# Kernel tuning notes

Measured on AMD Instinct MI355X. Metric: run time of the kernel, lower is better.

Reference implementation:

```python
import jax, jax.numpy as jnp
import numpy as np

B, S, D, H, DH, F = 2, 2048, 1024, 16, 64, 4096
K = 2048  # number of selected tokens (capacity_gamma=0.5 of B*S)
EPS = 1e-6
ROPE_THETA = 10000.0


def setup_inputs() -> dict:
    key = jax.random.key(0)
    ks = jax.random.split(key, 12)
    w = lambda k, shp: jax.random.normal(k, shp, dtype=jnp.float32) * 0.02
    # K unique flat indices into the B*S token grid (every other token -> unique, sorted)
    sel_flat = jnp.arange(K, dtype=jnp.int64) * 2
    return {
        "hidden_states": jax.random.normal(ks[0], (B, S, D), dtype=jnp.float32),
        "gating_signal": jax.random.uniform(ks[1], (B, S), dtype=jnp.float32),
        "sel_flat": sel_flat,
        "position_ids": jnp.tile(jnp.arange(S, dtype=jnp.int64), (B, 1)),
        "ln1_w": jnp.ones((D,), jnp.float32),
        "ln2_w": jnp.ones((D,), jnp.float32),
        "wq": w(ks[2], (D, H * DH)), "bq": jnp.zeros((H * DH,), jnp.float32),
        "wk": w(ks[3], (D, H * DH)), "bk": jnp.zeros((H * DH,), jnp.float32),
        "wv": w(ks[4], (D, H * DH)), "bv": jnp.zeros((H * DH,), jnp.float32),
        "wo": w(ks[5], (H * DH, D)),
        "w_gate": w(ks[6], (D, F)),
        "w_up": w(ks[7], (D, F)),
        "w_down": w(ks[8], (F, D)),
    }


def _rmsnorm(x, w):
    var = jnp.mean(jnp.square(x), axis=-1, keepdims=True)
    return x * jax.lax.rsqrt(var + EPS) * w


def _rope(x, pos):
    # x: [K, H, DH], pos: [K]
    half = DH // 2
    inv_freq = 1.0 / (ROPE_THETA ** (jnp.arange(half, dtype=jnp.float32) / half))
    ang = pos.astype(jnp.float32)[:, None] * inv_freq  # [K, half]
    cos = jnp.cos(ang)[:, None, :]
    sin = jnp.sin(ang)[:, None, :]
    x1, x2 = x[..., :half], x[..., half:]
    return jnp.concatenate([x1 * cos - x2 * sin, x2 * cos + x1 * sin], axis=-1)


def reference(hidden_states, gating_signal, sel_flat, position_ids,
              ln1_w, ln2_w, wq, bq, wk, bk, wv, bv, wo, w_gate, w_up, w_down):
    b_idx = sel_flat // S
    t_idx = sel_flat % S

    # --- gather selected tokens ---
    x = hidden_states[b_idx, t_idx]          # [K, D]
    g = gating_signal[b_idx, t_idx]          # [K]
    pos = position_ids[b_idx, t_idx]         # [K]

    # --- Qwen2 block on the selected tokens (single sequence of length K) ---
    h = _rmsnorm(x, ln1_w)
    q = _rope((h @ wq + bq).reshape(K, H, DH), pos)
    k = _rope((h @ wk + bk).reshape(K, H, DH), pos)
    v = (h @ wv + bv).reshape(K, H, DH)

    scores = jnp.einsum("qhd,khd->hqk", q, k) / np.sqrt(DH)  # [H, K, K]
    causal = jnp.tril(jnp.ones((K, K), dtype=bool))
    scores = jnp.where(causal, scores, jnp.finfo(scores.dtype).min)
    probs = jax.nn.softmax(scores, axis=-1)
    attn = jnp.einsum("hqk,khd->qhd", probs, v).reshape(K, H * DH) @ wo

    x1 = x + attn
    h2 = _rmsnorm(x1, ln2_w)
    mlp = (jax.nn.silu(h2 @ w_gate) * (h2 @ w_up)) @ w_down
    y = x1 + mlp                              # processed tokens [K, D]

    # --- gated residual scatter-back ---
    updated = x + (y - x) * g[:, None]
    return hidden_states.at[b_idx, t_idx].set(updated)
```

## Files before the change

### kernel.cpp

```cpp
#include <hip/hip_runtime.h>
#include <hip/hip_bf16.h>
#include <stdint.h>

#define K_TOK 2048
#define D_DIM 1024
#define H_N   16
#define DH_N  64
#define F_DIM 4096
#define S_SEQ 2048

typedef __attribute__((ext_vector_type(4))) float f32x4;
typedef __attribute__((ext_vector_type(8))) short bf16x8;

__device__ __forceinline__ float bf2f(ushort u) {
  union { unsigned u; float f; } c; c.u = ((unsigned)u) << 16; return c.f;
}
__device__ __forceinline__ ushort f2bf(float f) {
  union { float f; unsigned u; } c; c.f = f;
  unsigned x = c.u + 0x7fffu + ((c.u >> 16) & 1u);
  return (ushort)(x >> 16);
}

#define GLOAD_LDS16(GP, LP)                                                   \
  __builtin_amdgcn_global_load_lds(                                           \
      (const __attribute__((address_space(1))) unsigned int*)(GP),            \
      (__attribute__((address_space(3))) unsigned int*)(LP), 16, 0, 0)

__global__ void copy_out_k(const float4* __restrict__ src, float4* __restrict__ dst, int n4) {
  int idx = blockIdx.x * blockDim.x + threadIdx.x;
  int stride = gridDim.x * blockDim.x;
  for (; idx < n4; idx += stride) dst[idx] = src[idx];
}

__global__ void prep_bias(const float* __restrict__ bq, const float* __restrict__ bk,
                          const float* __restrict__ bv, float* __restrict__ dst) {
  int i = blockIdx.x * 256 + threadIdx.x;
  if (i < 3072) dst[i] = (i < 1024) ? bq[i] : (i < 2048 ? bk[i - 1024] : bv[i - 2048]);
}

__global__ __launch_bounds__(256) void transpose_conv64(const float* __restrict__ src,
                                                        ushort* __restrict__ dst,
                                                        int R, int C, int mul, int add, int ldd) {
  __shared__ float tile[64][65];
  int nbx = C >> 6;
  int bx = blockIdx.x % nbx, by = blockIdx.x / nbx;
  int c0 = bx << 6, r0 = by << 6;
  int tx = threadIdx.x & 15, ty = threadIdx.x >> 4;
#pragma unroll
  for (int i = 0; i < 4; ++i) {
    float4 v = *(const float4*)&src[(size_t)(r0 + ty + i * 16) * C + c0 + tx * 4];
    *(float4*)&tile[ty + i * 16][tx * 4] = v;
  }
  __syncthreads();
#pragma unroll
  for (int i = 0; i < 4; ++i) {
    int c = ty + i * 16;
    ushort4 o;
    o.x = f2bf(tile[tx * 4 + 0][c]);
    o.y = f2bf(tile[tx * 4 + 1][c]);
    o.z = f2bf(tile[tx * 4 + 2][c]);
    o.w = f2bf(tile[tx * 4 + 3][c]);
    *(ushort4*)&dst[(size_t)((c0 + c) * mul + add) * ldd + r0 + tx * 4] = o;
  }
}

__global__ __launch_bounds__(256) void gather_ln1(
    const float* __restrict__ hs, const float* __restrict__ gating,
    const int* __restrict__ sel32, const int* __restrict__ pos32,
    const float* __restrict__ w,
    float* __restrict__ xbuf, ushort* __restrict__ hbuf,
    float* __restrict__ gbuf, int* __restrict__ rowb, int* __restrict__ rowt,
    int* __restrict__ rowpos) {
  int i = blockIdx.x, tid = threadIdx.x;
  __shared__ float red[4];
  bool is64 = (sel32[1] == 0 && sel32[3] == 0 && sel32[5] == 0);
  int sel = is64 ? sel32[2 * i] : sel32[i];
  int b = sel >> 11;
  int t = sel & 2047;
  const float4* src = (const float4*)(hs + ((size_t)b * S_SEQ + t) * D_DIM);
  float4 v = src[tid];
  float ss = v.x * v.x + v.y * v.y + v.z * v.z + v.w * v.w;
  for (int off = 32; off; off >>= 1) ss += __shfl_xor(ss, off);
  if ((tid & 63) == 0) red[tid >> 6] = ss;
  __syncthreads();
  float tot = red[0] + red[1] + red[2] + red[3];
  float rms = rsqrtf(tot * (1.f / 1024.f) + 1e-6f);
  ((float4*)(xbuf + (size_t)i * D_DIM))[tid] = v;
  float4 lw = ((const float4*)w)[tid];
  ushort4 hv;
  hv.x = f2bf(v.x * rms * lw.x); hv.y = f2bf(v.y * rms * lw.y);
  hv.z = f2bf(v.z * rms * lw.z); hv.w = f2bf(v.w * rms * lw.w);
  *(ushort4*)&hbuf[(size_t)i * D_DIM + tid * 4] = hv;
  if (tid == 0) {
    rowb[i] = b; rowt[i] = t;
    bool is64p = (pos32[1] == 0 && pos32[3] == 0 && pos32[5] == 0);
    int pidx = b * S_SEQ + t;
    rowpos[i] = is64p ? pos32[2 * pidx] : pos32[pidx];
    gbuf[i] = gating[pidx];
  }
}

__global__ __launch_bounds__(256) void rmsnorm_ep1(const float* __restrict__ xbuf,
                                                   const float* __restrict__ pb,
                                                   const float* __restrict__ w,
                                                   float* __restrict__ x1out,
                                                   ushort* __restrict__ h2out) {
  int i = blockIdx.x, tid = threadIdx.x;
  __shared__ float red[4];
  size_t e = (size_t)i * D_DIM;
  float4 v = ((const float4*)(xbuf + e))[tid];
  float4 p0 = ((const float4*)(pb + e))[tid];
  float4 p1 = ((const float4*)(pb + 2097152 + e))[tid];
  v.x += p0.x + p1.x; v.y += p0.y + p1.y; v.z += p0.z + p1.z; v.w += p0.w + p1.w;
  ((float4*)(x1out + e))[tid] = v;
  float ss = v.x * v.x + v.y * v.y + v.z * v.z + v.w * v.w;
  for (int off = 32; off; off >>= 1) ss += __shfl_xor(ss, off);
  if ((tid & 63) == 0) red[tid >> 6] = ss;
  __syncthreads();
  float tot = red[0] + red[1] + red[2] + red[3];
  float rms = rsqrtf(tot * (1.f / 1024.f) + 1e-6f);
  float4 lw = ((const float4*)w)[tid];
  ushort4 hv;
  hv.x = f2bf(v.x * rms * lw.x); hv.y = f2bf(v.y * rms * lw.y);
  hv.z = f2bf(v.z * rms * lw.z); hv.w = f2bf(v.w * rms * lw.w);
  *(ushort4*)&h2out[e + tid * 4] = hv;
}

__global__ __launch_bounds__(256) void ep3_k(const float* __restrict__ pb,
                                             const float* __restrict__ x1b,
                                             const float* __restrict__ xbuf,
                                             const float* __restrict__ gbuf,
                                             const int* __restrict__ rowb,
                                             const int* __restrict__ rowt,
                                             float* __restrict__ out) {
  int idx = blockIdx.x * 256 + threadIdx.x;
  int row = idx >> 8, c4 = idx & 255;
  size_t e = (size_t)row * D_DIM + c4 * 4;
  float4 s0 = *(const float4*)(pb + e);
  float4 s1 = *(const float4*)(pb + 2097152 + e);
  float4 s2 = *(const float4*)(pb + 2 * 2097152 + e);
  float4 s3 = *(const float4*)(pb + 3 * 2097152 + e);
  float4 x = *(const float4*)(xbuf + e);
  float4 x1 = *(const float4*)(x1b + e);
  float g = gbuf[row];
  float4 r;
  r.x = x.x + (x1.x + s0.x + s1.x + s2.x + s3.x - x.x) * g;
  r.y = x.y + (x1.y + s0.y + s1.y + s2.y + s3.y - x.y) * g;
  r.z = x.z + (x1.z + s0.z + s1.z + s2.z + s3.z - x.z) * g;
  r.w = x.w + (x1.w + s0.w + s1.w + s2.w + s3.w - x.w) * g;
  *(float4*)(out + ((size_t)rowb[row] * S_SEQ + rowt[row]) * D_DIM + c4 * 4) = r;
}

template <int MODE>
__global__ __launch_bounds__(256) void gemm_bt(
    const ushort* __restrict__ A, const ushort* __restrict__ BT,
    int M, int N, int ldk, int kdeff, int per,
    const float* __restrict__ bias,
    ushort* __restrict__ outb, float* __restrict__ outf) {
  __shared__ ushort lA[128 * 64];
  __shared__ ushort lB[128 * 64];
  int tid = threadIdx.x;
  int lane = tid & 63, wid = tid >> 6;
  int kidx = blockIdx.x / per;
  int bid = blockIdx.x % per;
  int nbn = N >> 7;
  int tm = bid / nbn, tn = bid % nbn;
  int wr = wid >> 1, wc = wid & 1;
  f32x4 acc[4][4];
#pragma unroll
  for (int m = 0; m < 4; ++m)
#pragma unroll
    for (int n = 0; n < 4; ++n) acc[m][n] = (f32x4){0.f, 0.f, 0.f, 0.f};

  const ushort* Ab = A + (size_t)(tm * 128) * ldk + (size_t)kidx * kdeff;
  const ushort* Bb = BT + (size_t)(tn * 128) * ldk + (size_t)kidx * kdeff;
  int lr = lane & 15, lg = lane >> 4;
  int prow = lane >> 3;
  int pch = lane & 7;

  for (int k0 = 0; k0 < kdeff; k0 += 64) {
    __syncthreads();
#pragma unroll
    for (int p = 0; p < 4; ++p) {
      int row = p * 32 + wid * 8 + prow;
      int g = pch ^ (row & 7);
      GLOAD_LDS16(Ab + (size_t)row * ldk + k0 + g * 8, &lA[(p * 32 + wid * 8) * 64]);
      GLOAD_LDS16(Bb + (size_t)row * ldk + k0 + g * 8, &lB[(p * 32 + wid * 8) * 64]);
    }
    __syncthreads();
#pragma unroll
    for (int ks = 0; ks < 2; ++ks) {
      bf16x8 af[4], bfv[4];
#pragma unroll
      for (int m = 0; m < 4; ++m) {
        int row = wr * 64 + m * 16 + lr;
        af[m] = *(const bf16x8*)((const char*)lA + row * 128 +
                                 ((ks * 64 + lg * 16) ^ ((row & 7) << 4)));
      }
#pragma unroll
      for (int n = 0; n < 4; ++n) {
        int row = wc * 64 + n * 16 + lr;
        bfv[n] = *(const bf16x8*)((const char*)lB + row * 128 +
                                  ((ks * 64 + lg * 16) ^ ((row & 7) << 4)));
      }
#pragma unroll
      for (int m = 0; m < 4; ++m)
#pragma unroll
        for (int n = 0; n < 4; ++n)
          acc[m][n] = __builtin_amdgcn_mfma_f32_16x16x32_bf16(af[m], bfv[n], acc[m][n], 0, 0, 0);
    }
  }

#pragma unroll
  for (int m = 0; m < 4; ++m) {
#pragma unroll
    for (int n = 0; n < 4; ++n) {
#pragma unroll
      for (int r = 0; r < 4; ++r) {
        int gr = tm * 128 + wr * 64 + m * 16 + lg * 4 + r;
        int gc = tn * 128 + wc * 64 + n * 16 + lr;
        float val = acc[m][n][r];
        if (MODE == 0) {
          outb[(size_t)gr * N + gc] = f2bf(val + bias[gc]);
        } else {
          outf[((size_t)kidx * M + gr) * N + gc] = val;
        }
      }
    }
  }
}

__global__ __launch_bounds__(512, 2) void gemm256_gu(const ushort* __restrict__ A,
                                                     const ushort* __restrict__ BT,
                                                     ushort* __restrict__ outb) {
  __shared__ ushort lA[2][256 * 64];
  __shared__ ushort lB[2][256 * 64];
  int tid = threadIdx.x, lane = tid & 63, wid = tid >> 6;
  int bid = blockIdx.x;
  int tm = bid & 7, tn = bid >> 3;
  int wm = wid >> 2, wn = wid & 3;
  int lr = lane & 15, lg = lane >> 4;
  const ushort* Ab = A + (size_t)(tm * 256) * 1024;
  const ushort* Bb = BT + (size_t)(tn * 256) * 1024;

  f32x4 acc[8][4];
#pragma unroll
  for (int m = 0; m < 8; ++m)
#pragma unroll
    for (int n = 0; n < 4; ++n) acc[m][n] = (f32x4){0.f, 0.f, 0.f, 0.f};

  int grow = lane >> 3;
  int gsw = (lane & 7) ^ grow;

  auto STG = [&](int bi, int t) {
#pragma unroll
    for (int r = 0; r < 4; ++r) {
      int rb = wid * 4 + r;
      int row = rb * 8 + grow;
      GLOAD_LDS16(Ab + (size_t)row * 1024 + t * 64 + gsw * 8, &lA[bi][rb * 512]);
      GLOAD_LDS16(Bb + (size_t)row * 1024 + t * 64 + gsw * 8, &lB[bi][rb * 512]);
    }
  };

  STG(0, 0);
  STG(1, 1);
  asm volatile("s_waitcnt vmcnt(8)" ::: "memory");
  __builtin_amdgcn_s_barrier();

  for (int t = 0; t < 16; ++t) {
    int c = t & 1;
    const char* bA = (const char*)&lA[c][0];
    const char* bB = (const char*)&lB[c][0];
    bf16x8 bfr[4][2], afh[4][2];
#pragma unroll
    for (int n = 0; n < 4; ++n) {
      int row = wn * 64 + n * 16 + lr;
#pragma unroll
      for (int kk = 0; kk < 2; ++kk)
        bfr[n][kk] = *(const bf16x8*)(bB + row * 128 + ((kk * 64 + lg * 16) ^ ((lr & 7) << 4)));
    }
#pragma unroll
    for (int m = 0; m < 4; ++m) {
      int row = wm * 128 + m * 16 + lr;
#pragma unroll
      for (int kk = 0; kk < 2; ++kk)
        afh[m][kk] = *(const bf16x8*)(bA + row * 128 + ((kk * 64 + lg * 16) ^ ((lr & 7) << 4)));
    }
    __builtin_amdgcn_s_setprio(1);
#pragma unroll
    for (int m = 0; m < 4; ++m)
#pragma unroll
      for (int n = 0; n < 4; ++n)
#pragma unroll
        for (int kk = 0; kk < 2; ++kk)
          acc[m][n] = __builtin_amdgcn_mfma_f32_16x16x32_bf16(afh[m][kk], bfr[n][kk],
                                                              acc[m][n], 0, 0, 0);
    __builtin_amdgcn_s_setprio(0);
#pragma unroll
    for (int m = 0; m < 4; ++m) {
      int row = wm * 128 + 64 + m * 16 + lr;
#pragma unroll
      for (int kk = 0; kk < 2; ++kk)
        afh[m][kk] = *(const bf16x8*)(bA + row * 128 + ((kk * 64 + lg * 16) ^ ((lr & 7) << 4)));
    }
    asm volatile("s_waitcnt lgkmcnt(0)" ::: "memory");
    __builtin_amdgcn_s_barrier();
    if (t + 2 < 16) STG(c, t + 2);
    __builtin_amdgcn_sched_barrier(0);
    __builtin_amdgcn_s_setprio(1);
#pragma unroll
    for (int m = 0; m < 4; ++m)
#pragma unroll
      for (int n = 0; n < 4; ++n)
#pragma unroll
        for (int kk = 0; kk < 2; ++kk)
          acc[4 + m][n] = __builtin_amdgcn_mfma_f32_16x16x32_bf16(afh[m][kk], bfr[n][kk],
                                                                  acc[4 + m][n], 0, 0, 0);
    __builtin_amdgcn_s_setprio(0);
    if (t < 15) {
      if (t + 2 < 16)
        asm volatile("s_waitcnt vmcnt(8)" ::: "memory");
      else
        asm volatile("s_waitcnt vmcnt(0)" ::: "memory");
      __builtin_amdgcn_s_barrier();
    }
  }

#pragma unroll
  for (int m = 0; m < 8; ++m) {
#pragma unroll
    for (int n = 0; n < 4; ++n) {
#pragma unroll
      for (int r = 0; r < 4; ++r) {
        int gr = tm * 256 + wm * 128 + m * 16 + lg * 4 + r;
        int gc = tn * 256 + wn * 64 + n * 16 + lr;
        float val = acc[m][n][r];
        float other = __shfl_xor(val, 1);
        if (!(lane & 1)) {
          float g = val, u = other;
          float a = g / (1.f + __expf(-g)) * u;
          outb[(size_t)gr * (F_DIM) + (gc >> 1)] = f2bf(a);
        }
      }
    }
  }
}

__global__ __launch_bounds__(256) void rope_kernel(const ushort* __restrict__ qkv,
                                                   const int* __restrict__ rowpos,
                                                   ushort* __restrict__ qr,
                                                   ushort* __restrict__ kr) {
  int idx = blockIdx.x * 256 + threadIdx.x;
  int i = idx >> 9;
  int rem = idx & 511;
  int h = rem >> 5, d = rem & 31;
  float pos = (float)rowpos[i];
  float inv = __expf(-(float)d * (9.210340371976184f / 32.0f));
  float ang = pos * inv;
  float sn, cs;
  __sincosf(ang, &sn, &cs);
  size_t base = (size_t)i * 3072;
  float q1 = bf2f(qkv[base + h * 64 + d]);
  float q2 = bf2f(qkv[base + h * 64 + 32 + d]);
  float k1 = bf2f(qkv[base + 1024 + h * 64 + d]);
  float k2 = bf2f(qkv[base + 1024 + h * 64 + 32 + d]);
  size_t ob = ((size_t)h * K_TOK + i) * DH_N;
  qr[ob + d] = f2bf((q1 * cs - q2 * sn) * 0.125f);
  qr[ob + 32 + d] = f2bf((q2 * cs + q1 * sn) * 0.125f);
  kr[ob + d] = f2bf(k1 * cs - k2 * sn);
  kr[ob + 32 + d] = f2bf(k2 * cs + k1 * sn);
}

__global__ __launch_bounds__(256) void vtrans_k(const ushort* __restrict__ qkv,
                                                ushort* __restrict__ vt) {
  __shared__ ushort tile[32][33];
  int bx = blockIdx.x & 63, by = blockIdx.x >> 6;
  int i0 = bx << 5, c0 = by << 5;
  int tx = threadIdx.x & 31, ty = threadIdx.x >> 5;
#pragma unroll
  for (int j = 0; j < 32; j += 8)
    tile[ty + j][tx] = qkv[(size_t)(i0 + ty + j) * 3072 + 2048 + c0 + tx];
  __syncthreads();
#pragma unroll
  for (int j = 0; j < 32; j += 8)
    vt[(size_t)(c0 + ty + j) * K_TOK + i0 + tx] = tile[tx][ty + j];
}

__global__ __launch_bounds__(256) void attn_mfma(const ushort* __restrict__ qr,
                                                 const ushort* __restrict__ kr,
                                                 const ushort* __restrict__ vt,
                                                 ushort* __restrict__ ows,
                                                 float* __restrict__ mlws) {
  __shared__ ushort ktile[2][64 * 64];
  __shared__ ushort vtile[2][64 * 64];
  __shared__ ushort pbuf[4][16 * 64];
  int tid = threadIdx.x, lane = tid & 63, wid = tid >> 6;
  int bid = blockIdx.x;
  int h = bid / 144;
  int rem = 143 - (bid % 144);
  int g = 0;
  while (rem >= 2 * (g + 1) * (g + 2)) ++g;
  int rem2 = rem - 2 * g * (g + 1);
  int qt = (g << 2) + rem2 / (g + 1);
  int ci = rem2 % (g + 1);
  int slot = h * 144 + rem;
  int q0 = qt << 6;
  int t0 = ci << 2;
  int t1 = min(t0 + 3, qt);

  const ushort* Kh = kr + (size_t)h * K_TOK * DH_N;
  const ushort* Vh = vt + (size_t)h * DH_N * K_TOK;
  int lr = lane & 15, lg = lane >> 4;
  int qbase = q0 + wid * 16;

  bf16x8 qf[2];
  const ushort* Qp = qr + ((size_t)h * K_TOK + qbase + lr) * DH_N + lg * 8;
  qf[0] = *(const bf16x8*)(Qp);
  qf[1] = *(const bf16x8*)(Qp + 32);

  f32x4 oa[4];
  float mreg[4], lreg[4];
#pragma unroll
  for (int ct = 0; ct < 4; ++ct) oa[ct] = (f32x4){0.f, 0.f, 0.f, 0.f};
#pragma unroll
  for (int r = 0; r < 4; ++r) { mreg[r] = -1e30f; lreg[r] = 0.f; }

  char* pws = (char*)&pbuf[wid][0];
  int srow8 = lane >> 3, schunk = lane & 7;

  auto stage = [&](int bi, int kb) {
#pragma unroll
    for (int j = 0; j < 2; ++j) {
      int rbase = wid * 16 + j * 8;
      int row = rbase + srow8;
      int gch = schunk ^ (row & 7);
      GLOAD_LDS16(Kh + (size_t)(kb + row) * DH_N + gch * 8, &ktile[bi][rbase * 64]);
      GLOAD_LDS16(Vh + (size_t)row * K_TOK + kb + gch * 8, &vtile[bi][rbase * 64]);
    }
  };

  stage(0, t0 << 6);
  int cur = 0;
  for (int t = t0; t <= t1; ++t) {
    int kb = t << 6;
    __syncthreads();
    if (t < t1) stage(cur ^ 1, (t + 1) << 6);

    const char* kt = (const char*)&ktile[cur][0];
    const char* vtl = (const char*)&vtile[cur][0];

    f32x4 sa[4];
#pragma unroll
    for (int ct = 0; ct < 4; ++ct) sa[ct] = (f32x4){0.f, 0.f, 0.f, 0.f};
#pragma unroll
    for (int s = 0; s < 2; ++s) {
#pragma unroll
      for (int ct = 0; ct < 4; ++ct) {
        int row = ct * 16 + lr;
        bf16x8 kf = *(const bf16x8*)(kt + row * 128 + ((s * 64 + lg * 16) ^ ((row & 7) << 4)));
        sa[ct] = __builtin_amdgcn_mfma_f32_16x16x32_bf16(qf[s], kf, sa[ct], 0, 0, 0);
      }
    }

#pragma unroll
    for (int r = 0; r < 4; ++r) {
      int q = qbase + lg * 4 + r;
      int prow = lg * 4 + r;
      float sv[4];
      float mx = mreg[r];
#pragma unroll
      for (int ct = 0; ct < 4; ++ct) {
        int key = kb + ct * 16 + lr;
        float x = sa[ct][r];
        sv[ct] = (key <= q) ? x : -1e30f;
        mx = fmaxf(mx, sv[ct]);
      }
      mx = fmaxf(mx, __shfl_xor(mx, 1));
      mx = fmaxf(mx, __shfl_xor(mx, 2));
      mx = fmaxf(mx, __shfl_xor(mx, 4));
      mx = fmaxf(mx, __shfl_xor(mx, 8));
      float resc = __expf(mreg[r] - mx);
      float ps = 0.f;
#pragma unroll
      for (int ct = 0; ct < 4; ++ct) {
        float p = __expf(sv[ct] - mx);
        ps += p;
        *(ushort*)(pws + prow * 128 + ((ct * 32 + lr * 2) ^ ((prow & 7) << 4))) = f2bf(p);
      }
      ps += __shfl_xor(ps, 1);
      ps += __shfl_xor(ps, 2);
      ps += __shfl_xor(ps, 4);
      ps += __shfl_xor(ps, 8);
      lreg[r] = lreg[r] * resc + ps;
      mreg[r] = mx;
#pragma unroll
      for (int ct = 0; ct < 4; ++ct) oa[ct][r] *= resc;
    }

    bf16x8 pf[2];
#pragma unroll
    for (int s = 0; s < 2; ++s)
      pf[s] = *(const bf16x8*)(pws + lr * 128 + ((s * 64 + lg * 16) ^ ((lr & 7) << 4)));
#pragma unroll
    for (int s = 0; s < 2; ++s) {
#pragma unroll
      for (int ct = 0; ct < 4; ++ct) {
        int row = ct * 16 + lr;
        bf16x8 vf = *(const bf16x8*)(vtl + row * 128 + ((s * 64 + lg * 16) ^ ((row & 7) << 4)));
        oa[ct] = __builtin_amdgcn_mfma_f32_16x16x32_bf16(pf[s], vf, oa[ct], 0, 0, 0);
      }
    }
    cur ^= 1;
  }

#pragma unroll
  for (int ct = 0; ct < 4; ++ct) {
#pragma unroll
    for (int r = 0; r < 4; ++r) {
      int prow = wid * 16 + lg * 4 + r;
      ows[(size_t)slot * 4096 + prow * 64 + ct * 16 + lr] = f2bf(oa[ct][r]);
    }
  }
  if (lr == 0) {
#pragma unroll
    for (int r = 0; r < 4; ++r) {
      int prow = wid * 16 + lg * 4 + r;
      mlws[(size_t)slot * 128 + prow] = mreg[r];
      mlws[(size_t)slot * 128 + 64 + prow] = lreg[r];
    }
  }
}

__global__ __launch_bounds__(256) void attn_combine(const ushort* __restrict__ ows,
                                                    const float* __restrict__ mlws,
                                                    ushort* __restrict__ aout) {
  int bid = blockIdx.x;
  int h = bid & 15, qt = bid >> 4;
  int g = qt >> 2;
  int nc = g + 1;
  int base = h * 144 + 2 * g * (g + 1) + (qt & 3) * nc;
  int tid = threadIdx.x;
  int row = tid >> 2, c0 = (tid & 3) * 16;
  float M = -1e30f;
  for (int i = 0; i < nc; ++i)
    M = fmaxf(M, mlws[(size_t)(base + i) * 128 + row]);
  float L = 0.f;
  float acc[16];
#pragma unroll
  for (int j = 0; j < 16; ++j) acc[j] = 0.f;
  for (int i = 0; i < nc; ++i) {
    size_t sl = (size_t)(base + i);
    float w = __expf(mlws[sl * 128 + row] - M);
    L += mlws[sl * 128 + 64 + row] * w;
    const bf16x8* op = (const bf16x8*)(ows + sl * 4096 + row * 64 + c0);
    bf16x8 v0 = op[0], v1 = op[1];
#pragma unroll
    for (int j = 0; j < 8; ++j) acc[j] += bf2f(((ushort)v0[j])) * w;
#pragma unroll
    for (int j = 0; j < 8; ++j) acc[8 + j] += bf2f(((ushort)v1[j])) * w;
  }
  float inv = 1.f / L;
  int q = qt * 64 + row;
  ushort* dst = aout + (size_t)q * D_DIM + h * DH_N + c0;
#pragma unroll
  for (int j = 0; j < 16; ++j) dst[j] = f2bf(acc[j] * inv);
}

extern "C" void kernel_launch(void* const* d_in, const int* in_sizes, int n_in,
                              void* d_out, int out_size, void* d_ws, size_t ws_size,
                              hipStream_t stream) {
  const float* hs = (const float*)d_in[0];
  const float* gating = (const float*)d_in[1];
  const int* sel32 = (const int*)d_in[2];
  const int* pos32 = (const int*)d_in[3];
  const float* ln1w = (const float*)d_in[4];
  const float* ln2w = (const float*)d_in[5];
  const float* wq = (const float*)d_in[6];
  const float* bq = (const float*)d_in[7];
  const float* wk = (const float*)d_in[8];
  const float* bk = (const float*)d_in[9];
  const float* wv = (const float*)d_in[10];
  const float* bv = (const float*)d_in[11];
  const float* wo = (const float*)d_in[12];
  const float* wg = (const float*)d_in[13];
  const float* wu = (const float*)d_in[14];
  const float* wd = (const float*)d_in[15];
  float* out = (float*)d_out;

  char* wsb = (char*)d_ws;
  size_t off = 0;
  auto alloc = [&](size_t bytes) -> void* {
    void* p = wsb + off;
    off += (bytes + 255) & ~(size_t)255;
    return p;
  };
  ushort* qkvT = (ushort*)alloc(3072ull * 1024 * 2);
  ushort* woT = (ushort*)alloc(1024ull * 1024 * 2);
  ushort* guT = (ushort*)alloc(8192ull * 1024 * 2);
  ushort* wdT = (ushort*)alloc(1024ull * 4096 * 2);
  float* biasqkv = (float*)alloc(3072 * 4);
  float* xbuf = (float*)alloc(2048ull * 1024 * 4);
  ushort* hbuf = (ushort*)alloc(2048ull * 1024 * 2);
  ushort* qkv = (ushort*)alloc(2048ull * 3072 * 2);
  ushort* qrb = (ushort*)alloc(16ull * 2048 * 64 * 2);
  ushort* krb = (ushort*)alloc(16ull * 2048 * 64 * 2);
  ushort* vtb = (ushort*)alloc(16ull * 64 * 2048 * 2);
  ushort* aoutb = (ushort*)alloc(2048ull * 1024 * 2);
  float* pbuf = (float*)hbuf;
  float* x1b = (float*)alloc(2048ull * 1024 * 4);
  ushort* h2b = (ushort*)alloc(2048ull * 1024 * 2);
  ushort* actb = (ushort*)alloc(2048ull * 4096 * 2);
  ushort* aows = (ushort*)x1b;
  float* amlws = (float*)((char*)x1b + 2304ull * 4096 * 2);
  float* gbuf = (float*)alloc(2048 * 4);
  int* rowb = (int*)alloc(2048 * 4);
  int* rowt = (int*)alloc(2048 * 4);
  int* rowpos = (int*)alloc(2048 * 4);
  if (off > ws_size) return;

  copy_out_k<<<2048, 256, 0, stream>>>((const float4*)hs, (float4*)out, (2 * S_SEQ * D_DIM) / 4);
  prep_bias<<<12, 256, 0, stream>>>(bq, bk, bv, biasqkv);
  transpose_conv64<<<256, 256, 0, stream>>>(wq, qkvT, 1024, 1024, 1, 0, 1024);
  transpose_conv64<<<256, 256, 0, stream>>>(wk, qkvT + 1024 * 1024, 1024, 1024, 1, 0, 1024);
  transpose_conv64<<<256, 256, 0, stream>>>(wv, qkvT + 2048 * 1024, 1024, 1024, 1, 0, 1024);
  transpose_conv64<<<256, 256, 0, stream>>>(wo, woT, 1024, 1024, 1, 0, 1024);
  transpose_conv64<<<1024, 256, 0, stream>>>(wg, guT, 1024, 4096, 2, 0, 1024);
  transpose_conv64<<<1024, 256, 0, stream>>>(wu, guT, 1024, 4096, 2, 1, 1024);
  transpose_conv64<<<1024, 256, 0, stream>>>(wd, wdT, 4096, 1024, 1, 0, 4096);
  gather_ln1<<<2048, 256, 0, stream>>>(hs, gating, sel32, pos32, ln1w, xbuf, hbuf, gbuf, rowb,
                                       rowt, rowpos);
  gemm_bt<0><<<16 * 24, 256, 0, stream>>>(hbuf, qkvT, 2048, 3072, 1024, 1024, 16 * 24, biasqkv,
                                          qkv, nullptr);
  rope_kernel<<<4096, 256, 0, stream>>>(qkv, rowpos, qrb, krb);
  vtrans_k<<<2048, 256, 0, stream>>>(qkv, vtb);
  attn_mfma<<<16 * 144, 256, 0, stream>>>(qrb, krb, vtb, aows, amlws);
  attn_combine<<<512, 256, 0, stream>>>(aows, amlws, aoutb);
  gemm_bt<4><<<2 * 16 * 8, 256, 0, stream>>>(aoutb, woT, 2048, 1024, 1024, 512, 16 * 8, nullptr,
                                             nullptr, pbuf);
  rmsnorm_ep1<<<2048, 256, 0, stream>>>(xbuf, pbuf, ln2w, x1b, h2b);
  gemm256_gu<<<256, 512, 0, stream>>>(h2b, guT, actb);
  gemm_bt<4><<<4 * 16 * 8, 256, 0, stream>>>(actb, wdT, 2048, 1024, 4096, 1024, 16 * 8, nullptr,
                                             nullptr, pbuf);
  ep3_k<<<2048, 256, 0, stream>>>(pbuf, x1b, xbuf, gbuf, rowb, rowt, out);
}
```

Measured before the change: 218.6 us.

## Merge prep launches, double-buffer gemm_bt LDS, remap gate/up tile order

Folds the seven weight-transpose launches and the bias packing into one prep_all kernel. It also merges the output copy with gather/LN1 and RoPE with the V transpose, which removes several kernel launches and their tail gaps. gemm_bt now uses double-buffered LDS with async global-to-LDS prefetch two tiles ahead, split-k MFMA phases and setprio, so loads overlap with compute. The gemm256_gu block-to-tile mapping is changed, apparently to improve L2 reuse. The cost is double the LDS in gemm_bt, which may lower occupancy, plus more complex waitcnt logic.

```diff
diff --git a/kernel.cpp b/kernel.cpp
--- a/kernel.cpp
+++ b/kernel.cpp
@@ -26,24 +26,38 @@
       (const __attribute__((address_space(1))) unsigned int*)(GP),            \
       (__attribute__((address_space(3))) unsigned int*)(LP), 16, 0, 0)
 
-__global__ void copy_out_k(const float4* __restrict__ src, float4* __restrict__ dst, int n4) {
-  int idx = blockIdx.x * blockDim.x + threadIdx.x;
-  int stride = gridDim.x * blockDim.x;
-  for (; idx < n4; idx += stride) dst[idx] = src[idx];
-}
-
-__global__ void prep_bias(const float* __restrict__ bq, const float* __restrict__ bk,
-                          const float* __restrict__ bv, float* __restrict__ dst) {
-  int i = blockIdx.x * 256 + threadIdx.x;
-  if (i < 3072) dst[i] = (i < 1024) ? bq[i] : (i < 2048 ? bk[i - 1024] : bv[i - 2048]);
-}
-
-__global__ __launch_bounds__(256) void transpose_conv64(const float* __restrict__ src,
-                                                        ushort* __restrict__ dst,
-                                                        int R, int C, int mul, int add, int ldd) {
+__global__ __launch_bounds__(256) void prep_all(
+    const float* __restrict__ wq, const float* __restrict__ wk,
+    const float* __restrict__ wv, const float* __restrict__ wo,
+    const float* __restrict__ wg, const float* __restrict__ wu,
+    const float* __restrict__ wd, const float* __restrict__ bq,
+    const float* __restrict__ bk, const float* __restrict__ bv,
+    ushort* __restrict__ qkvT, ushort* __restrict__ woT,
+    ushort* __restrict__ guT, ushort* __restrict__ wdT,
+    float* __restrict__ biasqkv) {
   __shared__ float tile[64][65];
+  int b = blockIdx.x;
+  if (b >= 4096) {
+    int i = (b - 4096) * 256 + threadIdx.x;
+    if (i < 3072)
+      biasqkv[i] = (i < 1024) ? bq[i] : (i < 2048 ? bk[i - 1024] : bv[i - 2048]);
+    return;
+  }
+  const float* src;
+  ushort* dst;
+  int C, mul, add, ldd, tid_tile;
+  if (b < 1024) {
+    int seg = b >> 8; tid_tile = b & 255; C = 1024; mul = 1; add = 0; ldd = 1024;
+    if (seg == 0) { src = wq; dst = qkvT; }
+    else if (seg == 1) { src = wk; dst = qkvT + 1024 * 1024; }
+    else if (seg == 2) { src = wv; dst = qkvT + 2048 * 1024; }
+    else { src = wo; dst = woT; }
+  } else if (b < 2048) { src = wg; dst = guT; tid_tile = b - 1024; C = 4096; mul = 2; add = 0; ldd = 1024; }
+  else if (b < 3072) { src = wu; dst = guT; tid_tile = b - 2048; C = 4096; mul = 2; add = 1; ldd = 1024; }
+  else { src = wd; dst = wdT; tid_tile = b - 3072; C = 1024; mul = 1; add = 0; ldd = 4096; }
+
   int nbx = C >> 6;
-  int bx = blockIdx.x % nbx, by = blockIdx.x / nbx;
+  int bx = tid_tile % nbx, by = tid_tile / nbx;
   int c0 = bx << 6, r0 = by << 6;
   int tx = threadIdx.x & 15, ty = threadIdx.x >> 4;
 #pragma unroll
@@ -64,15 +78,21 @@
   }
 }
 
-__global__ __launch_bounds__(256) void gather_ln1(
+__global__ __launch_bounds__(256) void gather_copy(
     const float* __restrict__ hs, const float* __restrict__ gating,
     const int* __restrict__ sel32, const int* __restrict__ pos32,
-    const float* __restrict__ w,
+    const float* __restrict__ w, float* __restrict__ outc,
     float* __restrict__ xbuf, ushort* __restrict__ hbuf,
     float* __restrict__ gbuf, int* __restrict__ rowb, int* __restrict__ rowt,
     int* __restrict__ rowpos) {
-  int i = blockIdx.x, tid = threadIdx.x;
   __shared__ float red[4];
+  int tid = threadIdx.x;
+  if (blockIdx.x < 4096) {
+    int idx = blockIdx.x * 256 + tid;
+    ((float4*)outc)[idx] = ((const float4*)hs)[idx];
+    return;
+  }
+  int i = blockIdx.x - 4096;
   bool is64 = (sel32[1] == 0 && sel32[3] == 0 && sel32[5] == 0);
   int sel = is64 ? sel32[2 * i] : sel32[i];
   int b = sel >> 11;
@@ -157,8 +177,8 @@
     int M, int N, int ldk, int kdeff, int per,
     const float* __restrict__ bias,
     ushort* __restrict__ outb, float* __restrict__ outf) {
-  __shared__ ushort lA[128 * 64];
-  __shared__ ushort lB[128 * 64];
+  __shared__ ushort lA[2][128 * 64];
+  __shared__ ushort lB[2][128 * 64];
   int tid = threadIdx.x;
   int lane = tid & 63, wid = tid >> 6;
   int kidx = blockIdx.x / per;
@@ -177,37 +197,70 @@
   int lr = lane & 15, lg = lane >> 4;
   int prow = lane >> 3;
   int pch = lane & 7;
-
-  for (int k0 = 0; k0 < kdeff; k0 += 64) {
-    __syncthreads();
+  int nk = kdeff >> 6;
+
+  auto STG = [&](int bi, int t) {
 #pragma unroll
     for (int p = 0; p < 4; ++p) {
-      int row = p * 32 + wid * 8 + prow;
+      int rb = p * 32 + wid * 8;
+      int row = rb + prow;
       int g = pch ^ (row & 7);
-      GLOAD_LDS16(Ab + (size_t)row * ldk + k0 + g * 8, &lA[(p * 32 + wid * 8) * 64]);
-      GLOAD_LDS16(Bb + (size_t)row * ldk + k0 + g * 8, &lB[(p * 32 + wid * 8) * 64]);
-    }
-    __syncthreads();
-#pragma unroll
-    for (int ks = 0; ks < 2; ++ks) {
-      bf16x8 af[4], bfv[4];
-#pragma unroll
-      for (int m = 0; m < 4; ++m) {
-        int row = wr * 64 + m * 16 + lr;
-        af[m] = *(const bf16x8*)((const char*)lA + row * 128 +
-                                 ((ks * 64 + lg * 16) ^ ((row & 7) << 4)));
-      }
-#pragma unroll
-      for (int n = 0; n < 4; ++n) {
-        int row = wc * 64 + n * 16 + lr;
-        bfv[n] = *(const bf16x8*)((const char*)lB + row * 128 +
-                                  ((ks * 64 + lg * 16) ^ ((row & 7) << 4)));
-      }
-#pragma unroll
-      for (int m = 0; m < 4; ++m)
-#pragma unroll
-        for (int n = 0; n < 4; ++n)
-          acc[m][n] = __builtin_amdgcn_mfma_f32_16x16x32_bf16(af[m], bfv[n], acc[m][n], 0, 0, 0);
+      GLOAD_LDS16(Ab + (size_t)row * ldk + t * 64 + g * 8, &lA[bi][rb * 64]);
+      GLOAD_LDS16(Bb + (size_t)row * ldk + t * 64 + g * 8, &lB[bi][rb * 64]);
+    }
+  };
+
+  STG(0, 0);
+  STG(1, 1);
+  asm volatile("s_waitcnt vmcnt(8)" ::: "memory");
+  __builtin_amdgcn_s_barrier();
+
+  for (int t = 0; t < nk; ++t) {
+    int c = t & 1;
+    const char* bA = (const char*)&lA[c][0];
+    const char* bB = (const char*)&lB[c][0];
+    bf16x8 bfv[4][2], af[4];
+#pragma unroll
+    for (int n = 0; n < 4; ++n) {
+      int row = wc * 64 + n * 16 + lr;
+#pragma unroll
+      for (int kk = 0; kk < 2; ++kk)
+        bfv[n][kk] = *(const bf16x8*)(bB + row * 128 + ((kk * 64 + lg * 16) ^ ((row & 7) << 4)));
+    }
+#pragma unroll
+    for (int m = 0; m < 4; ++m) {
+      int row = wr * 64 + m * 16 + lr;
+      af[m] = *(const bf16x8*)(bA + row * 128 + ((lg * 16) ^ ((row & 7) << 4)));
+    }
+    __builtin_amdgcn_s_setprio(1);
+#pragma unroll
+    for (int m = 0; m < 4; ++m)
+#pragma unroll
+      for (int n = 0; n < 4; ++n)
+        acc[m][n] = __builtin_amdgcn_mfma_f32_16x16x32_bf16(af[m], bfv[n][0], acc[m][n], 0, 0, 0);
+    __builtin_amdgcn_s_setprio(0);
+#pragma unroll
+    for (int m = 0; m < 4; ++m) {
+      int row = wr * 64 + m * 16 + lr;
+      af[m] = *(const bf16x8*)(bA + row * 128 + ((64 + lg * 16) ^ ((row & 7) << 4)));
+    }
+    asm volatile("s_waitcnt lgkmcnt(0)" ::: "memory");
+    __builtin_amdgcn_s_barrier();
+    if (t + 2 < nk) STG(c, t + 2);
+    __builtin_amdgcn_sched_barrier(0);
+    __builtin_amdgcn_s_setprio(1);
+#pragma unroll
+    for (int m = 0; m < 4; ++m)
+#pragma unroll
+      for (int n = 0; n < 4; ++n)
+        acc[m][n] = __builtin_amdgcn_mfma_f32_16x16x32_bf16(af[m], bfv[n][1], acc[m][n], 0, 0, 0);
+    __builtin_amdgcn_s_setprio(0);
+    if (t < nk - 1) {
+      if (t + 2 < nk)
+        asm volatile("s_waitcnt vmcnt(8)" ::: "memory");
+      else
+        asm volatile("s_waitcnt vmcnt(0)" ::: "memory");
+      __builtin_amdgcn_s_barrier();
     }
   }
 
@@ -237,7 +290,8 @@
   __shared__ ushort lB[2][256 * 64];
   int tid = threadIdx.x, lane = tid & 63, wid = tid >> 6;
   int bid = blockIdx.x;
-  int tm = bid & 7, tn = bid >> 3;
+  int tn = (bid & 7) * 4 + ((bid >> 3) & 3);
+  int tm = bid >> 5;
   int wm = wid >> 2, wn = wid & 3;
   int lr = lane & 15, lg = lane >> 4;
   const ushort* Ab = A + (size_t)(tm * 256) * 1024;
@@ -346,35 +400,36 @@
   }
 }
 
-__global__ __launch_bounds__(256) void rope_kernel(const ushort* __restrict__ qkv,
+__global__ __launch_bounds__(256) void rope_vtrans(const ushort* __restrict__ qkv,
                                                    const int* __restrict__ rowpos,
                                                    ushort* __restrict__ qr,
-                                                   ushort* __restrict__ kr) {
-  int idx = blockIdx.x * 256 + threadIdx.x;
-  int i = idx >> 9;
-  int rem = idx & 511;
-  int h = rem >> 5, d = rem & 31;
-  float pos = (float)rowpos[i];
-  float inv = __expf(-(float)d * (9.210340371976184f / 32.0f));
-  float ang = pos * inv;
-  float sn, cs;
-  __sincosf(ang, &sn, &cs);
-  size_t base = (size_t)i * 3072;
-  float q1 = bf2f(qkv[base + h * 64 + d]);
-  float q2 = bf2f(qkv[base + h * 64 + 32 + d]);
-  float k1 = bf2f(qkv[base + 1024 + h * 64 + d]);
-  float k2 = bf2f(qkv[base + 1024 + h * 64 + 32 + d]);
-  size_t ob = ((size_t)h * K_TOK + i) * DH_N;
-  qr[ob + d] = f2bf((q1 * cs - q2 * sn) * 0.125f);
-  qr[ob + 32 + d] = f2bf((q2 * cs + q1 * sn) * 0.125f);
-  kr[ob + d] = f2bf(k1 * cs - k2 * sn);
-  kr[ob + 32 + d] = f2bf(k2 * cs + k1 * sn);
-}
-
-__global__ __launch_bounds__(256) void vtrans_k(const ushort* __restrict__ qkv,
-                                                ushort* __restrict__ vt) {
+                                                   ushort* __restrict__ kr,
+                                                   ushort* __restrict__ vt) {
   __shared__ ushort tile[32][33];
-  int bx = blockIdx.x & 63, by = blockIdx.x >> 6;
+  if (blockIdx.x < 4096) {
+    int idx = blockIdx.x * 256 + threadIdx.x;
+    int i = idx >> 9;
+    int rem = idx & 511;
+    int h = rem >> 5, d = rem & 31;
+    float pos = (float)rowpos[i];
+    float inv = __expf(-(float)d * (9.210340371976184f / 32.0f));
+    float ang = pos * inv;
+    float sn, cs;
+    __sincosf(ang, &sn, &cs);
+    size_t base = (size_t)i * 3072;
+    float q1 = bf2f(qkv[base + h * 64 + d]);
+    float q2 = bf2f(qkv[base + h * 64 + 32 + d]);
+    float k1 = bf2f(qkv[base + 1024 + h * 64 + d]);
+    float k2 = bf2f(qkv[base + 1024 + h * 64 + 32 + d]);
+    size_t ob = ((size_t)h * K_TOK + i) * DH_N;
+    qr[ob + d] = f2bf((q1 * cs - q2 * sn) * 0.125f);
+    qr[ob + 32 + d] = f2bf((q2 * cs + q1 * sn) * 0.125f);
+    kr[ob + d] = f2bf(k1 * cs - k2 * sn);
+    kr[ob + 32 + d] = f2bf(k2 * cs + k1 * sn);
+    return;
+  }
+  int bid = blockIdx.x - 4096;
+  int bx = bid & 63, by = bid >> 6;
   int i0 = bx << 5, c0 = by << 5;
   int tx = threadIdx.x & 31, ty = threadIdx.x >> 5;
 #pragma unroll
@@ -618,21 +673,13 @@
   int* rowpos = (int*)alloc(2048 * 4);
   if (off > ws_size) return;
 
-  copy_out_k<<<2048, 256, 0, stream>>>((const float4*)hs, (float4*)out, (2 * S_SEQ * D_DIM) / 4);
-  prep_bias<<<12, 256, 0, stream>>>(bq, bk, bv, biasqkv);
-  transpose_conv64<<<256, 256, 0, stream>>>(wq, qkvT, 1024, 1024, 1, 0, 1024);
-  transpose_conv64<<<256, 256, 0, stream>>>(wk, qkvT + 1024 * 1024, 1024, 1024, 1, 0, 1024);
-  transpose_conv64<<<256, 256, 0, stream>>>(wv, qkvT + 2048 * 1024, 1024, 1024, 1, 0, 1024);
-  transpose_conv64<<<256, 256, 0, stream>>>(wo, woT, 1024, 1024, 1, 0, 1024);
-  transpose_conv64<<<1024, 256, 0, stream>>>(wg, guT, 1024, 4096, 2, 0, 1024);
-  transpose_conv64<<<1024, 256, 0, stream>>>(wu, guT, 1024, 4096, 2, 1, 1024);
-  transpose_conv64<<<1024, 256, 0, stream>>>(wd, wdT, 4096, 1024, 1, 0, 4096);
-  gather_ln1<<<2048, 256, 0, stream>>>(hs, gating, sel32, pos32, ln1w, xbuf, hbuf, gbuf, rowb,
-                                       rowt, rowpos);
+  prep_all<<<4108, 256, 0, stream>>>(wq, wk, wv, wo, wg, wu, wd, bq, bk, bv, qkvT, woT, guT,
+                                     wdT, biasqkv);
+  gather_copy<<<6144, 256, 0, stream>>>(hs, gating, sel32, pos32, ln1w, out, xbuf, hbuf, gbuf,
+                                        rowb, rowt, rowpos);
   gemm_bt<0><<<16 * 24, 256, 0, stream>>>(hbuf, qkvT, 2048, 3072, 1024, 1024, 16 * 24, biasqkv,
                                           qkv, nullptr);
-  rope_kernel<<<4096, 256, 0, stream>>>(qkv, rowpos, qrb, krb);
-  vtrans_k<<<2048, 256, 0, stream>>>(qkv, vtb);
+  rope_vtrans<<<6144, 256, 0, stream>>>(qkv, rowpos, qrb, krb, vtb);
   attn_mfma<<<16 * 144, 256, 0, stream>>>(qrb, krb, vtb, aows, amlws);
   attn_combine<<<512, 256, 0, stream>>>(aows, amlws, aoutb);
   gemm_bt<4><<<2 * 16 * 8, 256, 0, stream>>>(aoutb, woT, 2048, 1024, 1024, 512, 16 * 8, nullptr,
```

Result: faster. 194.9 us (-10.8%).
